# Performance work log

Hardware: AMD Instinct MI355X
Metric: run time of the kernel (lower is better)

## Reference

```python
import jax, jax.numpy as jnp
import numpy as np

N_NODES = 50000
N_EDGES = 800000
C_FEAT = 96
HID = 96
C_CONST = 0.005


def _psi(v):
    return jnp.sign(v) * jnp.log(jnp.abs(v) + 1.0)


def setup_inputs() -> dict:
    key = jax.random.key(0)
    ks = jax.random.split(key, 16)
    d_e_in = 2 * C_FEAT + 2
    d_h_in = 2 * C_FEAT
    def w(k, fan_in, fan_out):
        return jax.random.normal(k, (fan_in, fan_out), jnp.float32) * (1.0 / np.sqrt(fan_in))
    return {
        "x": jax.random.normal(ks[0], (N_NODES, 4), jnp.float32),
        "h": jax.random.normal(ks[1], (N_NODES, C_FEAT), jnp.float32),
        "edge_i": jax.random.randint(ks[2], (N_EDGES,), 0, N_NODES, jnp.int32),
        "edge_j": jax.random.randint(ks[3], (N_EDGES,), 0, N_NODES, jnp.int32),
        "We1": w(ks[4], d_e_in, HID), "be1": jnp.zeros((HID,), jnp.float32),
        "We2": w(ks[5], HID, HID), "be2": jnp.zeros((HID,), jnp.float32),
        "Wm": w(ks[6], HID, 1), "bm": jnp.zeros((1,), jnp.float32),
        "Wh1": w(ks[7], d_h_in, HID), "bh1": jnp.zeros((HID,), jnp.float32),
        "Wh2": w(ks[8], HID, C_FEAT), "bh2": jnp.zeros((C_FEAT,), jnp.float32),
        "Wx1": w(ks[9], HID, HID), "bx1": jnp.zeros((HID,), jnp.float32),
        "Wx2": w(ks[10], HID, 1),  # bias-free last phi_x layer
    }


def reference(x, h, edge_i, edge_j, We1, be1, We2, be2, Wm, bm,
              Wh1, bh1, Wh2, bh2, Wx1, bx1, Wx2):
    n = x.shape[0]
    x_i = x[edge_i]            # (K,4)
    x_j = x[edge_j]            # (K,4)
    # Minkowski invariants: 2*t-component - full Euclidean sum == (+,-,-,-)
    d2 = jnp.square(x_i - x_j)
    norms = 2.0 * d2[..., 0] - jnp.sum(d2, axis=-1)
    z = x_i * x_j
    prods = 2.0 * z[..., 0] - jnp.sum(z, axis=-1)
    norms = _psi(norms)[:, None]   # (K,1)
    prods = _psi(prods)[:, None]   # (K,1)

    e_in = jnp.concatenate([h[edge_i], h[edge_j], norms, prods], axis=-1)  # (K,2C+2)
    m = jax.nn.relu(jax.nn.relu(e_in @ We1 + be1) @ We2 + be2)             # (K,HID)
    w_gate = jax.nn.sigmoid(m @ Wm + bm)                                   # (K,1)

    wm = jax.ops.segment_sum(w_gate * m, edge_i, num_segments=n)          # (N,HID)
    dh = jax.nn.relu(jnp.concatenate([h, wm], axis=-1) @ Wh1 + bh1) @ Wh2 + bh2
    h_out = h + dh

    phi_x = jax.nn.relu(m @ Wx1 + bx1) @ Wx2                              # (K,1)
    vals = phi_x * x_j                                                     # (K,4)
    s = jax.ops.segment_sum(vals, edge_i, num_segments=n)                 # (N,4)
    cnt = jax.ops.segment_sum(jnp.ones((vals.shape[0],), vals.dtype), edge_i, num_segments=n)
    mean = jnp.where(cnt[:, None] > 0, s / jnp.maximum(cnt[:, None], 1.0), 0.0)
    x_out = x + C_CONST * mean
    return (h_out, x_out)
```

## Files before the change

### kernel.cpp

```cpp
#include <hip/hip_runtime.h>
#include <math.h>

#define NN 50000
#define NE 800000
#define NB 196
#define TE 128

typedef __attribute__((ext_vector_type(8))) short short8v;
typedef __attribute__((ext_vector_type(4))) float f32x4;

__device__ __forceinline__ unsigned short f2bf(float f) {
  unsigned u = __float_as_uint(f);
  u += 0x7FFFu + ((u >> 16) & 1u);
  return (unsigned short)(u >> 16);
}
__device__ __forceinline__ unsigned pk2(float a, float b) {
  return (unsigned)f2bf(a) | ((unsigned)f2bf(b) << 16);
}
__device__ __forceinline__ float bflo(unsigned u) { return __uint_as_float(u << 16); }
__device__ __forceinline__ float bfhi(unsigned u) { return __uint_as_float(u & 0xFFFF0000u); }

__global__ void kprep(const int* __restrict__ ei, int* __restrict__ cnt,
                      const float* __restrict__ We1, const float* __restrict__ We2,
                      const float* __restrict__ Wx1, const float* __restrict__ Wh1,
                      const float* __restrict__ Wh2,
                      unsigned short* __restrict__ We1p, unsigned short* __restrict__ We2p,
                      unsigned short* __restrict__ Wx1p, unsigned short* __restrict__ Wh1p,
                      unsigned short* __restrict__ Wh2p) {
  const int b = blockIdx.x;
  if (b < NE / 256) {
    const int i = b * 256 + threadIdx.x;
    atomicAdd(&cnt[ei[i]], 1);
    return;
  }
  const int t = (b - NE / 256) * 256 + threadIdx.x;
  const int j = t & 7, lane = (t >> 3) & 63;
  const int kk = (lane >> 4) * 8 + j;
  const int nn = lane & 15;
  {
    const int tile = t >> 9, tk = tile / 12, tn = tile % 12;
    const int k = tk * 32 + kk, n2 = tn * 16 + nn;
    const float v = (n2 < 96) ? We1[k * 96 + n2] : We1[(96 + k) * 96 + (n2 - 96)];
    We1p[t] = f2bf(v);
  }
  {
    const int tile = t >> 9, tk = tile / 6, tn = tile % 6;
    const int k = tk * 32 + kk, n = tn * 16 + nn;
    Wh1p[t] = f2bf(Wh1[k * 96 + n]);
  }
  if (t < 9216) {
    const int tile = t >> 9, tk = tile / 6, tn = tile % 6;
    const int k = tk * 32 + kk, n = tn * 16 + nn;
    We2p[t] = f2bf(We2[k * 96 + n]);
    Wx1p[t] = f2bf(Wx1[k * 96 + n]);
    Wh2p[t] = f2bf(Wh2[k * 96 + n]);
  }
}

__global__ void kscanA(const int* __restrict__ cnt, int* __restrict__ pre,
                       int* __restrict__ bsum) {
  __shared__ int ps[256];
  const int b = blockIdx.x, t = threadIdx.x, idx = b * 256 + t;
  const int v = (idx < NN) ? cnt[idx] : 0;
  ps[t] = v;
  __syncthreads();
  for (int off = 1; off < 256; off <<= 1) {
    const int u = (t >= off) ? ps[t - off] : 0;
    __syncthreads();
    ps[t] += u;
    __syncthreads();
  }
  if (idx < NN) pre[idx] = ps[t] - v;
  if (t == 255) bsum[b] = ps[255];
}

__global__ void kscanBC(const int* __restrict__ pre, const int* __restrict__ bsum,
                        int* __restrict__ base, int* __restrict__ cursor) {
  __shared__ int ws[4];
  const int b = blockIdx.x, t = threadIdx.x;
  int s = (t < b) ? bsum[t] : 0;
  s += __shfl_xor(s, 1);  s += __shfl_xor(s, 2);  s += __shfl_xor(s, 4);
  s += __shfl_xor(s, 8);  s += __shfl_xor(s, 16); s += __shfl_xor(s, 32);
  if ((t & 63) == 0) ws[t >> 6] = s;
  __syncthreads();
  const int boff = ws[0] + ws[1] + ws[2] + ws[3];
  const int idx = b * 256 + t;
  if (idx < NN) {
    const int v = pre[idx] + boff;
    base[idx] = v;
    cursor[idx] = v;
  }
  if (idx == 0) base[NN] = NE;
}

__global__ void kperm(const int* __restrict__ ei, const int* __restrict__ ej,
                      int* __restrict__ cursor, int2* __restrict__ ep,
                      float* __restrict__ wz) {
  const int i = blockIdx.x * 256 + threadIdx.x;
  if (i < 625000) {
    const float4 z = make_float4(0.f, 0.f, 0.f, 0.f);
    *(float4*)(wz + (size_t)i * 8) = z;
    *(float4*)(wz + (size_t)i * 8 + 4) = z;
  }
  const int vi = ei[i];
  const int pos = atomicAdd(&cursor[vi], 1);
  ep[pos] = make_int2(vi, ej[i]);
}

__global__ __launch_bounds__(256, 4) void k0_AB(const float* __restrict__ h,
                                                const unsigned short* __restrict__ We1p,
                                                unsigned short* __restrict__ Abf,
                                                unsigned short* __restrict__ Bbf) {
  __shared__ __align__(16) unsigned short hbT[64 * 104];
  __shared__ __align__(16) unsigned short outT[64 * 200];
  const int tid = threadIdx.x;
  const int nb = blockIdx.x * 64;
  {
    const int e = tid & 63, q = tid >> 6;
    const int node = nb + e;
    const int nc = node < NN ? node : NN - 1;
    const float* hr = h + (long)nc * 96 + q * 24;
    unsigned* dst = (unsigned*)hbT + e * 52 + q * 12;
    #pragma unroll
    for (int c = 0; c < 6; ++c) {
      const float4 v = *(const float4*)(hr + c * 4);
      dst[c * 2]     = pk2(v.x, v.y);
      dst[c * 2 + 1] = pk2(v.z, v.w);
    }
  }
  __syncthreads();
  const int l = tid & 63, w = tid >> 6, cg = l & 15, rg = l >> 4;
  {
    const short8v* Wp = (const short8v*)We1p;
    const unsigned short* ar = hbT + (w * 16 + cg) * 104;
    const short8v af0 = *(const short8v*)(ar + rg * 8);
    const short8v af1 = *(const short8v*)(ar + 32 + rg * 8);
    const short8v af2 = *(const short8v*)(ar + 64 + rg * 8);
    #pragma unroll
    for (int tn = 0; tn < 12; ++tn) {
      f32x4 acc = (f32x4){0.f, 0.f, 0.f, 0.f};
      acc = __builtin_amdgcn_mfma_f32_16x16x32_bf16(af0, Wp[(0 * 12 + tn) * 64 + l], acc, 0, 0, 0);
      acc = __builtin_amdgcn_mfma_f32_16x16x32_bf16(af1, Wp[(1 * 12 + tn) * 64 + l], acc, 0, 0, 0);
      acc = __builtin_amdgcn_mfma_f32_16x16x32_bf16(af2, Wp[(2 * 12 + tn) * 64 + l], acc, 0, 0, 0);
      #pragma unroll
      for (int r = 0; r < 4; ++r)
        outT[(w * 16 + rg * 4 + r) * 200 + tn * 16 + cg] = f2bf(acc[r]);
    }
  }
  __syncthreads();
  {
    const int e = tid & 63, q = tid >> 6;
    const int node = nb + e;
    if (node < NN) {
      const unsigned* src = (const unsigned*)outT + e * 100;
      if (q < 2) {
        uint4* dA = (uint4*)(Abf + (size_t)node * 96);
        #pragma unroll
        for (int i = 0; i < 6; ++i) dA[q * 6 + i] = *(const uint4*)(src + (q * 6 + i) * 4);
      } else {
        uint4* dB = (uint4*)(Bbf + (size_t)node * 96);
        #pragma unroll
        for (int i = 0; i < 6; ++i) dB[(q - 2) * 6 + i] = *(const uint4*)(src + 48 + ((q - 2) * 6 + i) * 4);
      }
    }
  }
}

__global__ __launch_bounds__(256, 5) void k1_edge(const float* __restrict__ x,
    const unsigned short* __restrict__ Abf, const unsigned short* __restrict__ Bbf,
    const int2* __restrict__ ep,
    const float* __restrict__ We1, const float* __restrict__ be1,
    const unsigned short* __restrict__ We2p, const float* __restrict__ be2,
    const float* __restrict__ Wm, const float* __restrict__ bm,
    const unsigned short* __restrict__ Wx1p, const float* __restrict__ bx1,
    const float* __restrict__ Wx2,
    float* __restrict__ wmo, float* __restrict__ svo) {
  __shared__ __align__(16) unsigned short actT[TE * 104];
  __shared__ float gl[TE];
  __shared__ float phil[TE];
  __shared__ __align__(16) float xjl[TE * 4];
  __shared__ int vseq[TE + 2];
  __shared__ unsigned long long bmask[2];

  const int tid = threadIdx.x;
  const float bm0 = bm[0];
  const int tb = blockIdx.x * TE;

  {
    const int e2 = tid & 127, hf = tid >> 7;
    const int fb = hf * 48;
    const int2 v2 = ep[tb + e2];
    const int vi = v2.x, vj = v2.y;
    const float4 xi = *(const float4*)(x + (long)vi * 4);
    const float4 xj = *(const float4*)(x + (long)vj * 4);
    if (hf == 0) {
      vseq[1 + e2] = vi;
      *(float4*)(xjl + e2 * 4) = xj;
    }
    if (tid == 0) {
      vseq[0] = (tb > 0) ? ep[tb - 1].x : -1;
      vseq[TE + 1] = (tb + TE < NE) ? ep[tb + TE].x : -1;
    }
    const float d0 = xi.x - xj.x, d1 = xi.y - xj.y, d2 = xi.z - xj.z, d3 = xi.w - xj.w;
    const float nrm = d0 * d0 - d1 * d1 - d2 * d2 - d3 * d3;
    const float prd = xi.x * xj.x - xi.y * xj.y - xi.z * xj.z - xi.w * xj.w;
    const float pn = copysignf(logf(fabsf(nrm) + 1.f), nrm);
    const float pp = copysignf(logf(fabsf(prd) + 1.f), prd);
    const uint4* Ar = (const uint4*)(Abf + (size_t)vi * 96 + fb);
    const uint4* Br = (const uint4*)(Bbf + (size_t)vj * 96 + fb);
    const float* wA = We1 + 192 * 96 + fb;
    const float* wB = We1 + 193 * 96 + fb;
    const float* bE = be1 + fb;
    unsigned* arow = (unsigned*)actT + e2 * 52 + hf * 24;
    #pragma unroll
    for (int c = 0; c < 6; ++c) {
      const uint4 A4 = Ar[c], B4 = Br[c];
      const unsigned au[4] = {A4.x, A4.y, A4.z, A4.w};
      const unsigned bu[4] = {B4.x, B4.y, B4.z, B4.w};
      #pragma unroll
      for (int k2 = 0; k2 < 4; ++k2) {
        const int f = c * 8 + k2 * 2;
        const float lo = fmaxf(bflo(au[k2]) + bflo(bu[k2]) + pn * wA[f] + pp * wB[f] + bE[f], 0.f);
        const float hi = fmaxf(bfhi(au[k2]) + bfhi(bu[k2]) + pn * wA[f + 1] + pp * wB[f + 1] + bE[f + 1], 0.f);
        arow[c * 4 + k2] = pk2(lo, hi);
      }
    }
  }
  __syncthreads();

  if (tid < TE) {
    const int pred = (vseq[1 + tid] != vseq[2 + tid]) ? 1 : 0;
    const unsigned long long mk = __ballot(pred);
    if ((tid & 63) == 0) bmask[tid >> 6] = mk;
  }

  const int l = tid & 63, w = tid >> 6;
  const int cg = l & 15, rg = l >> 4;
  const int r0 = w * 32;
  const short8v* Wp2 = (const short8v*)We2p;
  const short8v* Wpx = (const short8v*)Wx1p;

  {
    short8v af[2][3];
    #pragma unroll
    for (int rt = 0; rt < 2; ++rt)
      #pragma unroll
      for (int tk = 0; tk < 3; ++tk)
        af[rt][tk] = *(const short8v*)(actT + (r0 + rt * 16 + cg) * 104 + tk * 32 + rg * 8);
    f32x4 acc[2][6];
    #pragma unroll
    for (int rt = 0; rt < 2; ++rt)
      #pragma unroll
      for (int tn = 0; tn < 6; ++tn) acc[rt][tn] = (f32x4){0.f, 0.f, 0.f, 0.f};
    #pragma unroll
    for (int tk = 0; tk < 3; ++tk)
      #pragma unroll
      for (int tn = 0; tn < 6; ++tn) {
        const short8v bf = Wp2[(tk * 6 + tn) * 64 + l];
        acc[0][tn] = __builtin_amdgcn_mfma_f32_16x16x32_bf16(af[0][tk], bf, acc[0][tn], 0, 0, 0);
        acc[1][tn] = __builtin_amdgcn_mfma_f32_16x16x32_bf16(af[1][tk], bf, acc[1][tn], 0, 0, 0);
      }
    #pragma unroll
    for (int rt = 0; rt < 2; ++rt) {
      float gp[4] = {0.f, 0.f, 0.f, 0.f};
      #pragma unroll
      for (int tn = 0; tn < 6; ++tn) {
        const int col = tn * 16 + cg;
        const float b = be2[col], wmw = Wm[col];
        #pragma unroll
        for (int r = 0; r < 4; ++r) {
          const float v = fmaxf(acc[rt][tn][r] + b, 0.f);
          gp[r] = fmaf(v, wmw, gp[r]);
          actT[(r0 + rt * 16 + rg * 4 + r) * 104 + col] = (unsigned short)f2bf(v);
        }
      }
      #pragma unroll
      for (int r = 0; r < 4; ++r) {
        float s = gp[r];
        s += __shfl_xor(s, 1); s += __shfl_xor(s, 2);
        s += __shfl_xor(s, 4); s += __shfl_xor(s, 8);
        if (cg == 0) gl[r0 + rt * 16 + rg * 4 + r] = 1.f / (1.f + expf(-(s + bm0)));
      }
    }
  }


  {
    short8v af[2][3];
    #pragma unroll
    for (int rt = 0; rt < 2; ++rt)
      #pragma unroll
      for (int tk = 0; tk < 3; ++tk)
        af[rt][tk] = *(const short8v*)(actT + (r0 + rt * 16 + cg) * 104 + tk * 32 + rg * 8);
    f32x4 acc[2][6];
    #pragma unroll
    for (int rt = 0; rt < 2; ++rt)
      #pragma unroll
      for (int tn = 0; tn < 6; ++tn) acc[rt][tn] = (f32x4){0.f, 0.f, 0.f, 0.f};
    #pragma unroll
    for (int tk = 0; tk < 3; ++tk)
      #pragma unroll
      for (int tn = 0; tn < 6; ++tn) {
        const short8v bf = Wpx[(tk * 6 + tn) * 64 + l];
        acc[0][tn] = __builtin_amdgcn_mfma_f32_16x16x32_bf16(af[0][tk], bf, acc[0][tn], 0, 0, 0);
        acc[1][tn] = __builtin_amdgcn_mfma_f32_16x16x32_bf16(af[1][tk], bf, acc[1][tn], 0, 0, 0);
      }
    #pragma unroll
    for (int rt = 0; rt < 2; ++rt) {
      float pp2[4] = {0.f, 0.f, 0.f, 0.f};
      #pragma unroll
      for (int tn = 0; tn < 6; ++tn) {
        const int col = tn * 16 + cg;
        const float b = bx1[col], wxw = Wx2[col];
        #pragma unroll
        for (int r = 0; r < 4; ++r)
          pp2[r] = fmaf(fmaxf(acc[rt][tn][r] + b, 0.f), wxw, pp2[r]);
      }
      #pragma unroll
      for (int r = 0; r < 4; ++r) {
        float s = pp2[r];
        s += __shfl_xor(s, 1); s += __shfl_xor(s, 2);
        s += __shfl_xor(s, 4); s += __shfl_xor(s, 8);
        if (cg == 0) phil[r0 + rt * 16 + rg * 4 + r] = s;
      }
    }
  }
  __syncthreads();

  if (tid < 192) {
    const int p = tid % 48;
    const int q = tid / 48;
    const int s_lo = q * 32;
    const unsigned long long mk = bmask[s_lo >> 6];
    float a0 = 0.f, a1 = 0.f;
    bool clean = (q == 0) ? (vseq[0] != vseq[1])
                          : (((bmask[(s_lo - 1) >> 6] >> ((s_lo - 1) & 63)) & 1ull) != 0);
    for (int i = 0; i < 32; ++i) {
      const int e = s_lo + i;
      const unsigned u = *(const unsigned*)(actT + e * 104 + 2 * p);
      const float g = gl[e];
      a0 = fmaf(g, bflo(u), a0);
      a1 = fmaf(g, bfhi(u), a1);
      const bool gend = ((mk >> (e & 63)) & 1ull) != 0;
      if (gend || i == 31) {
        const int node = vseq[e + 1];
        float* dst = wmo + (size_t)node * 96 + 2 * p;
        if (clean && gend) {
          *(float2*)dst = make_float2(a0, a1);
        } else {
          atomicAdd(dst, a0);
          atomicAdd(dst + 1, a1);
        }
        a0 = a1 = 0.f; clean = true;
      }
    }
  } else if (tid < 224) {
    const int t2 = tid - 192;
    const int comp = t2 & 3, q8 = t2 >> 2;
    const int s_lo = q8 * 16;
    const unsigned long long mk = bmask[s_lo >> 6];
    float acc2 = 0.f;
    bool clean = (q8 == 0) ? (vseq[0] != vseq[1])
                           : (((bmask[(s_lo - 1) >> 6] >> ((s_lo - 1) & 63)) & 1ull) != 0);
    for (int i = 0; i < 16; ++i) {
      const int e = s_lo + i;
      acc2 = fmaf(phil[e], xjl[e * 4 + comp], acc2);
      const bool gend = ((mk >> (e & 63)) & 1ull) != 0;
      if (gend || i == 15) {
        const int node = vseq[e + 1];
        float* dst = svo + (size_t)node * 4 + comp;
        if (clean && gend) *dst = acc2; else atomicAdd(dst, acc2);
        acc2 = 0.f; clean = true;
      }
    }
  }
}

__global__ __launch_bounds__(256, 4) void k3ab(const float* __restrict__ h,
    const float* __restrict__ wmv,
    const unsigned short* __restrict__ Wh1p, const float* __restrict__ bh1,
    const unsigned short* __restrict__ Wh2p, const float* __restrict__ bh2,
    const float* __restrict__ x, const float* __restrict__ svm,
    const int* __restrict__ basep,
    float* __restrict__ hout, float* __restrict__ xout) {
  __shared__ __align__(16) unsigned short inT[64 * 200];
  __shared__ __align__(16) unsigned short tmpT[64 * 104];
  const int tid = threadIdx.x;
  const int nb = blockIdx.x * 64;
  {
    const int e = tid & 63, q = tid >> 6;
    const int node = nb + e;
    const int nc = node < NN ? node : NN - 1;
    const float* hr = h + (long)nc * 96 + q * 24;
    const float* wr = wmv + (long)nc * 96 + q * 24;
    unsigned* dh = (unsigned*)inT + e * 100 + q * 12;
    unsigned* dw = (unsigned*)inT + e * 100 + 48 + q * 12;
    #pragma unroll
    for (int c = 0; c < 6; ++c) {
      const float4 v = *(const float4*)(hr + c * 4);
      dh[c * 2]     = pk2(v.x, v.y);
      dh[c * 2 + 1] = pk2(v.z, v.w);
      const float4 u = *(const float4*)(wr + c * 4);
      dw[c * 2]     = pk2(u.x, u.y);
      dw[c * 2 + 1] = pk2(u.z, u.w);
    }
  }
  __syncthreads();
  const int l = tid & 63, w = tid >> 6, cg = l & 15, rg = l >> 4;
  {
    const unsigned short* ar = inT + (w * 16 + cg) * 200;
    short8v af[6];
    #pragma unroll
    for (int tk = 0; tk < 6; ++tk) af[tk] = *(const short8v*)(ar + tk * 32 + rg * 8);
    const short8v* Wp = (const short8v*)Wh1p;
    #pragma unroll
    for (int tn = 0; tn < 6; ++tn) {
      f32x4 acc = (f32x4){0.f, 0.f, 0.f, 0.f};
      #pragma unroll
      for (int tk = 0; tk < 6; ++tk)
        acc = __builtin_amdgcn_mfma_f32_16x16x32_bf16(af[tk], Wp[(tk * 6 + tn) * 64 + l], acc, 0, 0, 0);
      const int col = tn * 16 + cg;
      const float b = bh1[col];
      #pragma unroll
      for (int r = 0; r < 4; ++r)
        tmpT[(w * 16 + rg * 4 + r) * 104 + col] = f2bf(fmaxf(acc[r] + b, 0.f));
    }
  }
  __syncthreads();
  {
    float* oT = (float*)inT;
    const unsigned short* mr = tmpT + (w * 16 + cg) * 104;
    const short8v mf0 = *(const short8v*)(mr + rg * 8);
    const short8v mf1 = *(const short8v*)(mr + 32 + rg * 8);
    const short8v mf2 = *(const short8v*)(mr + 64 + rg * 8);
    const short8v* Wp = (const short8v*)Wh2p;
    #pragma unroll
    for (int tn = 0; tn < 6; ++tn) {
      f32x4 acc = (f32x4){0.f, 0.f, 0.f, 0.f};
      acc = __builtin_amdgcn_mfma_f32_16x16x32_bf16(mf0, Wp[(0 * 6 + tn) * 64 + l], acc, 0, 0, 0);
      acc = __builtin_amdgcn_mfma_f32_16x16x32_bf16(mf1, Wp[(1 * 6 + tn) * 64 + l], acc, 0, 0, 0);
      acc = __builtin_amdgcn_mfma_f32_16x16x32_bf16(mf2, Wp[(2 * 6 + tn) * 64 + l], acc, 0, 0, 0);
      const int col = tn * 16 + cg;
      const float b = bh2[col];
      #pragma unroll
      for (int r = 0; r < 4; ++r)
        oT[(w * 16 + rg * 4 + r) * 100 + col] = acc[r] + b;
    }
  }
  __syncthreads();
  {
    const int e = tid & 63, q = tid >> 6;
    const int node = nb + e;
    if (node < NN) {
      const float* src = (const float*)inT + e * 100 + q * 24;
      const float* hr = h + (size_t)node * 96 + q * 24;
      float* dst = hout + (size_t)node * 96 + q * 24;
      #pragma unroll
      for (int c = 0; c < 6; ++c) {
        const float4 s = *(const float4*)(src + c * 4);
        const float4 hv = *(const float4*)(hr + c * 4);
        *(float4*)(dst + c * 4) = make_float4(hv.x + s.x, hv.y + s.y, hv.z + s.z, hv.w + s.w);
      }
    }
  }
  if (tid < 64) {
    const int node = nb + tid;
    if (node < NN) {
      const int cnt = basep[node + 1] - basep[node];
      const float inv = cnt > 0 ? 1.f / (float)cnt : 0.f;
      const float4 s4 = *(const float4*)(svm + (long)node * 4);
      const float4 xv = *(const float4*)(x + (long)node * 4);
      *(float4*)(xout + (long)node * 4) =
          make_float4(xv.x + 0.005f * s4.x * inv, xv.y + 0.005f * s4.y * inv,
                      xv.z + 0.005f * s4.z * inv, xv.w + 0.005f * s4.w * inv);
    }
  }
}

extern "C" void kernel_launch(void* const* d_in, const int* in_sizes, int n_in,
                              void* d_out, int out_size, void* d_ws, size_t ws_size,
                              hipStream_t stream) {
  const float* x   = (const float*)d_in[0];
  const float* h   = (const float*)d_in[1];
  const int*   ei  = (const int*)d_in[2];
  const int*   ej  = (const int*)d_in[3];
  const float* We1 = (const float*)d_in[4];
  const float* be1 = (const float*)d_in[5];
  const float* We2 = (const float*)d_in[6];
  const float* be2 = (const float*)d_in[7];
  const float* Wm  = (const float*)d_in[8];
  const float* bm  = (const float*)d_in[9];
  const float* Wh1 = (const float*)d_in[10];
  const float* bh1 = (const float*)d_in[11];
  const float* Wh2 = (const float*)d_in[12];
  const float* bh2 = (const float*)d_in[13];
  const float* Wx1 = (const float*)d_in[14];
  const float* bx1 = (const float*)d_in[15];
  const float* Wx2 = (const float*)d_in[16];

  char* w = (char*)d_ws;
  unsigned short* Abf  = (unsigned short*)w;
  unsigned short* Bbf  = (unsigned short*)(w + 9600000);
  float* WMv  = (float*)(w + 19200000);
  float* SvM  = (float*)(w + 38400000);
  int*   cnt  = (int*)(w + 39200000);
  int*   base = (int*)(w + 39400000);
  int*   curs = (int*)(w + 39600064);
  unsigned short* We2p = (unsigned short*)(w + 39800064);
  unsigned short* Wx1p = (unsigned short*)(w + 39818496);
  unsigned short* We1p = (unsigned short*)(w + 39836928);
  unsigned short* Wh1p = (unsigned short*)(w + 39873792);
  unsigned short* Wh2p = (unsigned short*)(w + 39910656);
  int2*  epb  = (int2*)(w + 39929088);
  int*   pre  = (int*)(w + 46329088);
  int*   bsum = (int*)(w + 46529088);

  float* hout = (float*)d_out;
  float* xout = hout + 4800000;

  hipMemsetAsync(cnt, 0, NN * sizeof(int), stream);
  kprep<<<NE / 256 + 72, 256, 0, stream>>>(ei, cnt, We1, We2, Wx1, Wh1, Wh2,
                                           We1p, We2p, Wx1p, Wh1p, Wh2p);
  kscanA<<<NB, 256, 0, stream>>>(cnt, pre, bsum);
  kscanBC<<<NB, 256, 0, stream>>>(pre, bsum, base, curs);
  kperm<<<NE / 256, 256, 0, stream>>>(ei, ej, curs, epb, WMv);
  k0_AB<<<782, 256, 0, stream>>>(h, We1p, Abf, Bbf);
  k1_edge<<<NE / TE, 256, 0, stream>>>(x, Abf, Bbf, epb, We1, be1, We2p, be2,
                                       Wm, bm, Wx1p, bx1, Wx2, WMv, SvM);
  k3ab<<<782, 256, 0, stream>>>(h, WMv, Wh1p, bh1, Wh2p, bh2, x, SvM, base, hout, xout);
}
```

Before: 280.7 us.

## Build first-layer edge activations directly in MFMA fragment registers, fold bias into node precompute

```diff
diff --git a/kernel.cpp b/kernel.cpp
--- a/kernel.cpp
+++ b/kernel.cpp
@@ -109,6 +109,7 @@
 
 __global__ __launch_bounds__(256, 4) void k0_AB(const float* __restrict__ h,
                                                 const unsigned short* __restrict__ We1p,
+                                                const float* __restrict__ be1,
                                                 unsigned short* __restrict__ Abf,
                                                 unsigned short* __restrict__ Bbf) {
   __shared__ __align__(16) unsigned short hbT[64 * 104];
@@ -142,9 +143,10 @@
       acc = __builtin_amdgcn_mfma_f32_16x16x32_bf16(af0, Wp[(0 * 12 + tn) * 64 + l], acc, 0, 0, 0);
       acc = __builtin_amdgcn_mfma_f32_16x16x32_bf16(af1, Wp[(1 * 12 + tn) * 64 + l], acc, 0, 0, 0);
       acc = __builtin_amdgcn_mfma_f32_16x16x32_bf16(af2, Wp[(2 * 12 + tn) * 64 + l], acc, 0, 0, 0);
+      const float bb = (tn < 6) ? be1[tn * 16 + cg] : 0.f;
       #pragma unroll
       for (int r = 0; r < 4; ++r)
-        outT[(w * 16 + rg * 4 + r) * 200 + tn * 16 + cg] = f2bf(acc[r]);
+        outT[(w * 16 + rg * 4 + r) * 200 + tn * 16 + cg] = f2bf(acc[r] + bb);
     }
   }
   __syncthreads();
@@ -169,7 +171,7 @@
 __global__ __launch_bounds__(256, 5) void k1_edge(const float* __restrict__ x,
     const unsigned short* __restrict__ Abf, const unsigned short* __restrict__ Bbf,
     const int2* __restrict__ ep,
-    const float* __restrict__ We1, const float* __restrict__ be1,
+    const float* __restrict__ We1,
     const unsigned short* __restrict__ We2p, const float* __restrict__ be2,
     const float* __restrict__ Wm, const float* __restrict__ bm,
     const unsigned short* __restrict__ Wx1p, const float* __restrict__ bx1,
@@ -179,51 +181,31 @@
   __shared__ float gl[TE];
   __shared__ float phil[TE];
   __shared__ __align__(16) float xjl[TE * 4];
+  __shared__ float pnl[TE], ppl[TE];
   __shared__ int vseq[TE + 2];
+  __shared__ int vjl[TE];
   __shared__ unsigned long long bmask[2];
 
   const int tid = threadIdx.x;
   const float bm0 = bm[0];
   const int tb = blockIdx.x * TE;
 
-  {
-    const int e2 = tid & 127, hf = tid >> 7;
-    const int fb = hf * 48;
-    const int2 v2 = ep[tb + e2];
+  if (tid < TE) {
+    const int2 v2 = ep[tb + tid];
     const int vi = v2.x, vj = v2.y;
+    vseq[1 + tid] = vi;
+    vjl[tid] = vj;
     const float4 xi = *(const float4*)(x + (long)vi * 4);
     const float4 xj = *(const float4*)(x + (long)vj * 4);
-    if (hf == 0) {
-      vseq[1 + e2] = vi;
-      *(float4*)(xjl + e2 * 4) = xj;
-    }
+    *(float4*)(xjl + tid * 4) = xj;
+    const float d0 = xi.x - xj.x, d1 = xi.y - xj.y, d2 = xi.z - xj.z, d3 = xi.w - xj.w;
+    const float nrm = d0 * d0 - d1 * d1 - d2 * d2 - d3 * d3;
+    const float prd = xi.x * xj.x - xi.y * xj.y - xi.z * xj.z - xi.w * xj.w;
+    pnl[tid] = copysignf(logf(fabsf(nrm) + 1.f), nrm);
+    ppl[tid] = copysignf(logf(fabsf(prd) + 1.f), prd);
     if (tid == 0) {
       vseq[0] = (tb > 0) ? ep[tb - 1].x : -1;
       vseq[TE + 1] = (tb + TE < NE) ? ep[tb + TE].x : -1;
-    }
-    const float d0 = xi.x - xj.x, d1 = xi.y - xj.y, d2 = xi.z - xj.z, d3 = xi.w - xj.w;
-    const float nrm = d0 * d0 - d1 * d1 - d2 * d2 - d3 * d3;
-    const float prd = xi.x * xj.x - xi.y * xj.y - xi.z * xj.z - xi.w * xj.w;
-    const float pn = copysignf(logf(fabsf(nrm) + 1.f), nrm);
-    const float pp = copysignf(logf(fabsf(prd) + 1.f), prd);
-    const uint4* Ar = (const uint4*)(Abf + (size_t)vi * 96 + fb);
-    const uint4* Br = (const uint4*)(Bbf + (size_t)vj * 96 + fb);
-    const float* wA = We1 + 192 * 96 + fb;
-    const float* wB = We1 + 193 * 96 + fb;
-    const float* bE = be1 + fb;
-    unsigned* arow = (unsigned*)actT + e2 * 52 + hf * 24;
-    #pragma unroll
-    for (int c = 0; c < 6; ++c) {
-      const uint4 A4 = Ar[c], B4 = Br[c];
-      const unsigned au[4] = {A4.x, A4.y, A4.z, A4.w};
-      const unsigned bu[4] = {B4.x, B4.y, B4.z, B4.w};
-      #pragma unroll
-      for (int k2 = 0; k2 < 4; ++k2) {
-        const int f = c * 8 + k2 * 2;
-        const float lo = fmaxf(bflo(au[k2]) + bflo(bu[k2]) + pn * wA[f] + pp * wB[f] + bE[f], 0.f);
-        const float hi = fmaxf(bfhi(au[k2]) + bfhi(bu[k2]) + pn * wA[f + 1] + pp * wB[f + 1] + bE[f + 1], 0.f);
-        arow[c * 4 + k2] = pk2(lo, hi);
-      }
     }
   }
   __syncthreads();
@@ -243,10 +225,36 @@
   {
     short8v af[2][3];
     #pragma unroll
-    for (int rt = 0; rt < 2; ++rt)
-      #pragma unroll
-      for (int tk = 0; tk < 3; ++tk)
-        af[rt][tk] = *(const short8v*)(actT + (r0 + rt * 16 + cg) * 104 + tk * 32 + rg * 8);
+    for (int rt = 0; rt < 2; ++rt) {
+      const int e = r0 + rt * 16 + cg;
+      const int vi = vseq[1 + e], vj = vjl[e];
+      const float pn = pnl[e], pp = ppl[e];
+      #pragma unroll
+      for (int tk = 0; tk < 3; ++tk) {
+        const int fb = tk * 32 + rg * 8;
+        const uint4 a4 = *(const uint4*)(Abf + (size_t)vi * 96 + fb);
+        const uint4 b4 = *(const uint4*)(Bbf + (size_t)vj * 96 + fb);
+        const float* wA = We1 + 192 * 96 + fb;
+        const float* wB = We1 + 193 * 96 + fb;
+        const unsigned au[4] = {a4.x, a4.y, a4.z, a4.w};
+        const unsigned bu[4] = {b4.x, b4.y, b4.z, b4.w};
+        unsigned pkd[4];
+        #pragma unroll
+        for (int p = 0; p < 4; ++p) {
+          const int f = 2 * p;
+          const float lo = fmaxf(bflo(au[p]) + bflo(bu[p]) + pn * wA[f] + pp * wB[f], 0.f);
+          const float hi = fmaxf(bfhi(au[p]) + bfhi(bu[p]) + pn * wA[f + 1] + pp * wB[f + 1], 0.f);
+          pkd[p] = pk2(lo, hi);
+        }
+        short8v fr;
+        fr[0] = (short)(pkd[0] & 0xFFFF); fr[1] = (short)(pkd[0] >> 16);
+        fr[2] = (short)(pkd[1] & 0xFFFF); fr[3] = (short)(pkd[1] >> 16);
+        fr[4] = (short)(pkd[2] & 0xFFFF); fr[5] = (short)(pkd[2] >> 16);
+        fr[6] = (short)(pkd[3] & 0xFFFF); fr[7] = (short)(pkd[3] >> 16);
+        af[rt][tk] = fr;
+      }
+    }
+
     f32x4 acc[2][6];
     #pragma unroll
     for (int rt = 0; rt < 2; ++rt)
@@ -524,8 +532,8 @@
   kscanA<<<NB, 256, 0, stream>>>(cnt, pre, bsum);
   kscanBC<<<NB, 256, 0, stream>>>(pre, bsum, base, curs);
   kperm<<<NE / 256, 256, 0, stream>>>(ei, ej, curs, epb, WMv);
-  k0_AB<<<782, 256, 0, stream>>>(h, We1p, Abf, Bbf);
-  k1_edge<<<NE / TE, 256, 0, stream>>>(x, Abf, Bbf, epb, We1, be1, We2p, be2,
+  k0_AB<<<782, 256, 0, stream>>>(h, We1p, be1, Abf, Bbf);
+  k1_edge<<<NE / TE, 256, 0, stream>>>(x, Abf, Bbf, epb, We1, We2p, be2,
                                        Wm, bm, Wx1p, bx1, Wx2, WMv, SvM);
   k3ab<<<782, 256, 0, stream>>>(h, WMv, Wh1p, bh1, Wh2p, bh2, x, SvM, base, hout, xout);
 }
```

Result: slower. 310.0 us (+10.4%).
